# Performance work log

Measured on AMD Instinct MI355X. Metric: run time of the kernel, lower is better.

The kernel has to match this reference:

```python
import jax, jax.numpy as jnp
import numpy as np
import math

N_EMBD = 1024
N_HEAD = 16
BLOCK_SIZE = 2048
B, T = 2, 2048

def setup_inputs() -> dict:
    key = jax.random.key(0)
    ks = jax.random.split(key, 5)
    x = jax.random.normal(ks[0], (B, T, N_EMBD), dtype=jnp.float32)
    s = 1.0 / math.sqrt(N_EMBD)
    W_attn = jax.random.normal(ks[1], (N_EMBD, 3 * N_EMBD), dtype=jnp.float32) * s
    b_attn = jnp.zeros((3 * N_EMBD,), dtype=jnp.float32)
    W_proj = jax.random.normal(ks[2], (N_EMBD, N_EMBD), dtype=jnp.float32) * s
    b_proj = jnp.zeros((N_EMBD,), dtype=jnp.float32)
    return {"x": x, "W_attn": W_attn, "b_attn": b_attn, "W_proj": W_proj, "b_proj": b_proj}

def reference(x, W_attn, b_attn, W_proj, b_proj):
    Bx, Tx, C = x.shape
    hd = C // N_HEAD  # head dim
    a = x @ W_attn + b_attn                     # [B,T,3C]
    q, k, v = jnp.split(a, 3, axis=2)
    # [B,T,C] -> [B,H,T,hd]
    q = q.reshape(Bx, Tx, N_HEAD, hd).transpose(0, 2, 1, 3)
    k = k.reshape(Bx, Tx, N_HEAD, hd).transpose(0, 2, 1, 3)
    v = v.reshape(Bx, Tx, N_HEAD, hd).transpose(0, 2, 1, 3)
    # NOTE: nonstandard scale from the source: 1/sqrt(3*n_embd // n_head)
    scale = 1.0 / math.sqrt(C * 3 // N_HEAD)
    attn = jnp.einsum('bhqd,bhkd->bhqk', q, k) * scale
    causal = jnp.tril(jnp.ones((Tx, Tx), dtype=bool))
    attn = jnp.where(causal[None, None, :, :], attn, -jnp.inf)
    attn = jax.nn.softmax(attn, axis=-1)
    y = jnp.einsum('bhqk,bhkd->bhqd', attn, v)
    y = y.transpose(0, 2, 1, 3).reshape(Bx, Tx, C)
    return y @ W_proj + b_proj
```

## Files before the change

### kernel.cpp

```cpp
#include <hip/hip_runtime.h>
#include <hip/hip_bf16.h>

typedef unsigned short u16;
typedef __attribute__((ext_vector_type(8))) short frag8;
typedef __attribute__((ext_vector_type(4))) float f32x4;

#define DEV __device__ __forceinline__

DEV float b2f(u16 u) {
  unsigned int x = ((unsigned int)u) << 16;
  return __builtin_bit_cast(float, x);
}
DEV u16 f2b(float f) {
  unsigned int x = __builtin_bit_cast(unsigned int, f);
  x += 0x7fffu + ((x >> 16) & 1u);
  return (u16)(x >> 16);
}

DEV void gload_lds16(const u16* g, u16* l) {
  __builtin_amdgcn_global_load_lds(
      (const __attribute__((address_space(1))) unsigned int*)g,
      (__attribute__((address_space(3))) unsigned int*)l, 16, 0, 0);
}

__global__ void cvt_x(const float* __restrict__ x, u16* __restrict__ xb,
                      int n4) {
  int i = blockIdx.x * blockDim.x + threadIdx.x;
  if (i < n4) {
    float4 v = ((const float4*)x)[i];
    ushort4 o;
    o.x = f2b(v.x); o.y = f2b(v.y); o.z = f2b(v.z); o.w = f2b(v.w);
    ((ushort4*)xb)[i] = o;
  }
}

__global__ void cvt_wt(const float* __restrict__ W, u16* __restrict__ Wt,
                       int K, int N) {
  __shared__ u16 tile[32][33];
  const int nb = blockIdx.x * 32, kb = blockIdx.y * 32;
  const int tx = threadIdx.x, ty = threadIdx.y;
#pragma unroll
  for (int j = 0; j < 4; j++)
    tile[ty + j * 8][tx] = f2b(W[(size_t)(kb + ty + j * 8) * N + nb + tx]);
  __syncthreads();
#pragma unroll
  for (int j = 0; j < 4; j++)
    Wt[(size_t)(nb + ty + j * 8) * K + kb + tx] = tile[tx][ty + j * 8];
}

constexpr int BM = 128, BN = 128, BK = 32;

template <int MODE>
__launch_bounds__(256)
__global__ void gemm_bt(const u16* __restrict__ A, const u16* __restrict__ Bt,
                        const float* __restrict__ bias,
                        u16* __restrict__ o0, u16* __restrict__ o1,
                        u16* __restrict__ o2, float* __restrict__ of,
                        int M, int N, int K) {
  __shared__ __align__(16) u16 As[BM * BK];
  __shared__ __align__(16) u16 Bs[BN * BK];
  const int tid = threadIdx.x;
  const int lane = tid & 63;
  const int wid = tid >> 6;
  const int m0 = blockIdx.y * BM;
  const int n0 = blockIdx.x * BN;
  const int wm = (wid >> 1) * 64;
  const int wn = (wid & 1) * 64;

  f32x4 acc[4][4] = {};

  const int ldr0 = wid * 16 + (lane >> 2);
  const int ldr1 = ldr0 + 64;
  const int ldk = (lane & 3) * 8;
  const u16* Ag0 = A + (size_t)(m0 + ldr0) * K + ldk;
  const u16* Ag1 = A + (size_t)(m0 + ldr1) * K + ldk;
  const u16* Bg0 = Bt + (size_t)(n0 + ldr0) * K + ldk;
  const u16* Bg1 = Bt + (size_t)(n0 + ldr1) * K + ldk;
  u16* lA0 = &As[(wid * 16) * BK];
  u16* lA1 = &As[(wid * 16 + 64) * BK];
  u16* lB0 = &Bs[(wid * 16) * BK];
  u16* lB1 = &Bs[(wid * 16 + 64) * BK];

  const int lr = lane & 15, lg = lane >> 4;

  for (int k0 = 0; k0 < K; k0 += BK) {
    gload_lds16(Ag0 + k0, lA0);
    gload_lds16(Ag1 + k0, lA1);
    gload_lds16(Bg0 + k0, lB0);
    gload_lds16(Bg1 + k0, lB1);
    __syncthreads();
    frag8 af[4], bf[4];
#pragma unroll
    for (int i = 0; i < 4; i++) {
      af[i] = *(const frag8*)&As[(wm + i * 16 + lr) * BK + lg * 8];
      bf[i] = *(const frag8*)&Bs[(wn + i * 16 + lr) * BK + lg * 8];
    }
#pragma unroll
    for (int mi = 0; mi < 4; mi++)
#pragma unroll
      for (int ni = 0; ni < 4; ni++)
        acc[mi][ni] = __builtin_amdgcn_mfma_f32_16x16x32_bf16(
            af[mi], bf[ni], acc[mi][ni], 0, 0, 0);
    __syncthreads();
  }

#pragma unroll
  for (int ni = 0; ni < 4; ni++) {
    const int n = n0 + wn + ni * 16 + lr;
    const float bv = bias[n];
#pragma unroll
    for (int mi = 0; mi < 4; mi++) {
      const int mr = m0 + wm + mi * 16 + lg * 4;
#pragma unroll
      for (int r = 0; r < 4; r++) {
        const float v = acc[mi][ni][r] + bv;
        const int m = mr + r;
        if (MODE == 1) {
          of[(size_t)m * N + n] = v;
        } else {
          const int sec = n >> 10, c = n & 1023, hh = c >> 6, dd = c & 63;
          const int bb = m >> 11, tt = m & 2047;
          if (sec == 0)
            o0[(((size_t)bb * 16 + hh) * 2048 + tt) * 64 + dd] = f2b(v);
          else if (sec == 1)
            o1[(((size_t)bb * 16 + hh) * 2048 + tt) * 64 + dd] = f2b(v);
          else
            o2[(((size_t)bb * 16 + hh) * 64 + dd) * 2048 + tt] = f2b(v);
        }
      }
    }
  }
}

__launch_bounds__(256)
__global__ void attn_fwd(const u16* __restrict__ Qg, const u16* __restrict__ Kg,
                         const u16* __restrict__ Vtg, u16* __restrict__ Og) {
  __shared__ __align__(16) u16 Kl[2][4096];
  __shared__ __align__(16) u16 Vl[2][4096];
  __shared__ __align__(16) u16 P_lds[4][16][72];
  const int tid = threadIdx.x, lane = tid & 63, wid = tid >> 6;
  const int bid = blockIdx.x;
  const int hb = bid & 31;
  const int pa = bid >> 5;
  const int h = hb & 15, b = hb >> 4;
  const size_t bh = (size_t)b * 16 + h;
  const u16* Qp = Qg + bh * 2048 * 64;
  const u16* Kp = Kg + bh * 2048 * 64;
  const u16* Vp = Vtg + bh * 64 * 2048;
  const int lr = lane & 15, lg = lane >> 4;
  const float scale = 0.07216878364870322f;

  frag8 vone;
#pragma unroll
  for (int i = 0; i < 8; i++) vone[i] = (short)0x3F80;

  int srow[2], scol[2];
#pragma unroll
  for (int c = 0; c < 2; c++) {
    const int sb = c * 4096 + tid * 16;
    const int row = sb >> 7;
    const int cs = (sb >> 4) & 7;
    srow[c] = row;
    scol[c] = ((cs ^ (row & 7)) << 3);
  }
  const int ldsoff0 = wid * 512;
  const int ldsoff1 = 2048 + wid * 512;

  for (int ph = 0; ph < 2; ++ph) {
    const int qblk = ph ? (31 - pa) : pa;
    const int nkv = qblk + 1;
    const int q0 = qblk * 64 + wid * 16;

    frag8 qf[2];
#pragma unroll
    for (int ks = 0; ks < 2; ks++)
      qf[ks] = *(const frag8*)&Qp[(size_t)(q0 + lr) * 64 + ks * 32 + lg * 8];

    f32x4 o[4] = {};
    f32x4 ls = {};

    gload_lds16(Kp + (size_t)(0 + srow[0]) * 64 + scol[0], &Kl[0][ldsoff0]);
    gload_lds16(Kp + (size_t)(0 + srow[1]) * 64 + scol[1], &Kl[0][ldsoff1]);
    gload_lds16(Vp + (size_t)srow[0] * 2048 + 0 + scol[0], &Vl[0][ldsoff0]);
    gload_lds16(Vp + (size_t)srow[1] * 2048 + 0 + scol[1], &Vl[0][ldsoff1]);
    __syncthreads();

    for (int kt = 0; kt < nkv; ++kt) {
      const int cur = kt & 1;
      if (kt + 1 < nkv) {
        const int kv1 = (kt + 1) << 6;
        u16* Kd = Kl[cur ^ 1];
        u16* Vd = Vl[cur ^ 1];
        gload_lds16(Kp + (size_t)(kv1 + srow[0]) * 64 + scol[0], Kd + ldsoff0);
        gload_lds16(Kp + (size_t)(kv1 + srow[1]) * 64 + scol[1], Kd + ldsoff1);
        gload_lds16(Vp + (size_t)srow[0] * 2048 + kv1 + scol[0], Vd + ldsoff0);
        gload_lds16(Vp + (size_t)srow[1] * 2048 + kv1 + scol[1], Vd + ldsoff1);
      }
      const u16* Kc = Kl[cur];
      const u16* Vc = Vl[cur];
      f32x4 s[4] = {};
#pragma unroll
      for (int ks = 0; ks < 2; ks++)
#pragma unroll
        for (int ni = 0; ni < 4; ni++) {
          const frag8 kf = *(const frag8*)&Kc[(ni * 16 + lr) * 64 +
                                              (((ks * 4 + lg) ^ (lr & 7)) << 3)];
          s[ni] = __builtin_amdgcn_mfma_f32_16x16x32_bf16(qf[ks], kf, s[ni], 0,
                                                          0, 0);
        }
      const bool last = (kt == nkv - 1);
#pragma unroll
      for (int r = 0; r < 4; r++) {
#pragma unroll
        for (int ni = 0; ni < 4; ni++) {
          float sv = s[ni][r] * scale;
          if (last)
            sv = (ni * 16 + lr <= wid * 16 + lg * 4 + r) ? sv
                                                         : -__builtin_inff();
          P_lds[wid][lg * 4 + r][ni * 16 + lr] = f2b(__expf(sv));
        }
      }
      asm volatile("s_waitcnt lgkmcnt(0)" ::: "memory");
#pragma unroll
      for (int ks = 0; ks < 2; ks++) {
        const frag8 pf = *(const frag8*)&P_lds[wid][lr][ks * 32 + lg * 8];
        ls = __builtin_amdgcn_mfma_f32_16x16x32_bf16(pf, vone, ls, 0, 0, 0);
#pragma unroll
        for (int di = 0; di < 4; di++) {
          const frag8 vfr = *(const frag8*)&Vc[(di * 16 + lr) * 64 +
                                               (((ks * 4 + lg) ^ (lr & 7))
                                                << 3)];
          o[di] = __builtin_amdgcn_mfma_f32_16x16x32_bf16(pf, vfr, o[di], 0, 0,
                                                          0);
        }
      }
      __syncthreads();
    }

#pragma unroll
    for (int r = 0; r < 4; r++) {
      const int t = q0 + lg * 4 + r;
      const float inv = 1.f / ls[r];
#pragma unroll
      for (int di = 0; di < 4; di++) {
        const int col = (h << 6) + di * 16 + lr;
        Og[((size_t)b * 2048 + t) * 1024 + col] = f2b(o[di][r] * inv);
      }
    }
  }
}

extern "C" void kernel_launch(void* const* d_in, const int* in_sizes, int n_in,
                              void* d_out, int out_size, void* d_ws,
                              size_t ws_size, hipStream_t stream) {
  const float* x = (const float*)d_in[0];
  const float* Wa = (const float*)d_in[1];
  const float* ba = (const float*)d_in[2];
  const float* Wp = (const float*)d_in[3];
  const float* bp = (const float*)d_in[4];
  float* out = (float*)d_out;
  u16* ws = (u16*)d_ws;

  u16* WtA = ws;
  u16* WtP = WtA + (size_t)3072 * 1024;
  u16* Qb = WtP + (size_t)1024 * 1024;
  u16* Kb = Qb + (size_t)4194304;
  u16* Vt = Kb + (size_t)4194304;
  u16* Ob = Vt + (size_t)4194304;
  u16* xb = Ob + (size_t)4194304;

  cvt_x<<<4096, 256, 0, stream>>>(x, xb, 1048576);
  cvt_wt<<<dim3(96, 32), dim3(32, 8), 0, stream>>>(Wa, WtA, 1024, 3072);
  cvt_wt<<<dim3(32, 32), dim3(32, 8), 0, stream>>>(Wp, WtP, 1024, 1024);
  gemm_bt<0><<<dim3(24, 32), 256, 0, stream>>>(xb, WtA, ba, Qb, Kb, Vt,
                                               nullptr, 4096, 3072, 1024);
  attn_fwd<<<512, 256, 0, stream>>>(Qb, Kb, Vt, Ob);
  gemm_bt<1><<<dim3(8, 32), 256, 0, stream>>>(Ob, WtP, bp, nullptr, nullptr,
                                              nullptr, out, 4096, 1024, 1024);
}
```

Baseline: 201.9 us.

## Swizzle GEMM LDS layout, merge conversion kernels, add smaller-tile projection GEMM

Applies an XOR swizzle to the k-column chunk used for global-to-LDS loads and fragment reads in the GEMM, so that LDS reads hit fewer bank conflicts. Merges the three fp32-to-bf16 conversion launches into one kernel to cut launch overhead. Adds a dedicated output-projection GEMM with 64x128 tiles, which doubles the block count to 512 so more of the GPU is occupied. In exchange the projection tiles get less data reuse, and the merged kernel branches on block index.

```diff
diff --git a/kernel.cpp b/kernel.cpp
--- a/kernel.cpp
+++ b/kernel.cpp
@@ -23,22 +23,32 @@
       (__attribute__((address_space(3))) unsigned int*)l, 16, 0, 0);
 }
 
-__global__ void cvt_x(const float* __restrict__ x, u16* __restrict__ xb,
-                      int n4) {
-  int i = blockIdx.x * blockDim.x + threadIdx.x;
-  if (i < n4) {
+__global__ void cvt_all(const float* __restrict__ x, u16* __restrict__ xb,
+                        const float* __restrict__ Wa, u16* __restrict__ WtA,
+                        const float* __restrict__ Wp, u16* __restrict__ WtP) {
+  const int bid = blockIdx.x, tid = threadIdx.x;
+  if (bid < 4096) {
+    const int i = bid * 256 + tid;
     float4 v = ((const float4*)x)[i];
     ushort4 o;
     o.x = f2b(v.x); o.y = f2b(v.y); o.z = f2b(v.z); o.w = f2b(v.w);
     ((ushort4*)xb)[i] = o;
-  }
-}
-
-__global__ void cvt_wt(const float* __restrict__ W, u16* __restrict__ Wt,
-                       int K, int N) {
+    return;
+  }
   __shared__ u16 tile[32][33];
-  const int nb = blockIdx.x * 32, kb = blockIdx.y * 32;
-  const int tx = threadIdx.x, ty = threadIdx.y;
+  const float* W;
+  u16* Wt;
+  int nb, kb, K, N;
+  if (bid < 7168) {
+    const int b2 = bid - 4096;
+    W = Wa; Wt = WtA; K = 1024; N = 3072;
+    nb = (b2 % 96) * 32; kb = (b2 / 96) * 32;
+  } else {
+    const int b3 = bid - 7168;
+    W = Wp; Wt = WtP; K = 1024; N = 1024;
+    nb = (b3 % 32) * 32; kb = (b3 / 32) * 32;
+  }
+  const int tx = tid & 31, ty = tid >> 5;
 #pragma unroll
   for (int j = 0; j < 4; j++)
     tile[ty + j * 8][tx] = f2b(W[(size_t)(kb + ty + j * 8) * N + nb + tx]);
@@ -71,7 +81,8 @@
 
   const int ldr0 = wid * 16 + (lane >> 2);
   const int ldr1 = ldr0 + 64;
-  const int ldk = (lane & 3) * 8;
+  const int f0 = (lane >> 3) & 3;
+  const int ldk = (((lane & 3) ^ f0) << 3);
   const u16* Ag0 = A + (size_t)(m0 + ldr0) * K + ldk;
   const u16* Ag1 = A + (size_t)(m0 + ldr1) * K + ldk;
   const u16* Bg0 = Bt + (size_t)(n0 + ldr0) * K + ldk;
@@ -82,6 +93,8 @@
   u16* lB1 = &Bs[(wid * 16 + 64) * BK];
 
   const int lr = lane & 15, lg = lane >> 4;
+  const int fr = (lr >> 1) & 3;
+  const int rcol = ((lg ^ fr) << 3);
 
   for (int k0 = 0; k0 < K; k0 += BK) {
     gload_lds16(Ag0 + k0, lA0);
@@ -92,8 +105,8 @@
     frag8 af[4], bf[4];
 #pragma unroll
     for (int i = 0; i < 4; i++) {
-      af[i] = *(const frag8*)&As[(wm + i * 16 + lr) * BK + lg * 8];
-      bf[i] = *(const frag8*)&Bs[(wn + i * 16 + lr) * BK + lg * 8];
+      af[i] = *(const frag8*)&As[(wm + i * 16 + lr) * BK + rcol];
+      bf[i] = *(const frag8*)&Bs[(wn + i * 16 + lr) * BK + rcol];
     }
 #pragma unroll
     for (int mi = 0; mi < 4; mi++)
@@ -128,6 +141,71 @@
             o2[(((size_t)bb * 16 + hh) * 64 + dd) * 2048 + tt] = f2b(v);
         }
       }
+    }
+  }
+}
+
+__launch_bounds__(256)
+__global__ void gemm_proj(const u16* __restrict__ A, const u16* __restrict__ Bt,
+                          const float* __restrict__ bias,
+                          float* __restrict__ of, int M, int N, int K) {
+  __shared__ __align__(16) u16 As[64 * 32];
+  __shared__ __align__(16) u16 Bs[128 * 32];
+  const int tid = threadIdx.x;
+  const int lane = tid & 63;
+  const int wid = tid >> 6;
+  const int m0 = blockIdx.y * 64;
+  const int n0 = blockIdx.x * 128;
+  const int wm = (wid >> 1) * 32;
+  const int wn = (wid & 1) * 64;
+
+  f32x4 acc[2][4] = {};
+
+  const int srow = tid >> 2;
+  const int f0 = (srow >> 1) & 3;
+  const int scol = (((tid & 3) ^ f0) << 3);
+  const u16* Ag = A + (size_t)(m0 + srow) * K + scol;
+  const u16* Bg0 = Bt + (size_t)(n0 + srow) * K + scol;
+  const u16* Bg1 = Bt + (size_t)(n0 + srow + 64) * K + scol;
+  u16* lA = &As[wid * 512];
+  u16* lB0 = &Bs[wid * 512];
+  u16* lB1 = &Bs[2048 + wid * 512];
+
+  const int lr = lane & 15, lg = lane >> 4;
+  const int fr = (lr >> 1) & 3;
+  const int rcol = ((lg ^ fr) << 3);
+
+  for (int k0 = 0; k0 < K; k0 += 32) {
+    gload_lds16(Ag + k0, lA);
+    gload_lds16(Bg0 + k0, lB0);
+    gload_lds16(Bg1 + k0, lB1);
+    __syncthreads();
+    frag8 af[2], bf[4];
+#pragma unroll
+    for (int i = 0; i < 2; i++)
+      af[i] = *(const frag8*)&As[(wm + i * 16 + lr) * 32 + rcol];
+#pragma unroll
+    for (int i = 0; i < 4; i++)
+      bf[i] = *(const frag8*)&Bs[(wn + i * 16 + lr) * 32 + rcol];
+#pragma unroll
+    for (int mi = 0; mi < 2; mi++)
+#pragma unroll
+      for (int ni = 0; ni < 4; ni++)
+        acc[mi][ni] = __builtin_amdgcn_mfma_f32_16x16x32_bf16(
+            af[mi], bf[ni], acc[mi][ni], 0, 0, 0);
+    __syncthreads();
+  }
+
+#pragma unroll
+  for (int ni = 0; ni < 4; ni++) {
+    const int n = n0 + wn + ni * 16 + lr;
+    const float bv = bias[n];
+#pragma unroll
+    for (int mi = 0; mi < 2; mi++) {
+      const int mr = m0 + wm + mi * 16 + lg * 4;
+#pragma unroll
+      for (int r = 0; r < 4; r++)
+        of[(size_t)(mr + r) * N + n] = acc[mi][ni][r] + bv;
     }
   }
 }
@@ -269,12 +347,10 @@
   u16* Ob = Vt + (size_t)4194304;
   u16* xb = Ob + (size_t)4194304;
 
-  cvt_x<<<4096, 256, 0, stream>>>(x, xb, 1048576);
-  cvt_wt<<<dim3(96, 32), dim3(32, 8), 0, stream>>>(Wa, WtA, 1024, 3072);
-  cvt_wt<<<dim3(32, 32), dim3(32, 8), 0, stream>>>(Wp, WtP, 1024, 1024);
+  cvt_all<<<8192, 256, 0, stream>>>(x, xb, Wa, WtA, Wp, WtP);
   gemm_bt<0><<<dim3(24, 32), 256, 0, stream>>>(xb, WtA, ba, Qb, Kb, Vt,
                                                nullptr, 4096, 3072, 1024);
   attn_fwd<<<512, 256, 0, stream>>>(Qb, Kb, Vt, Ob);
-  gemm_bt<1><<<dim3(8, 32), 256, 0, stream>>>(Ob, WtP, bp, nullptr, nullptr,
-                                              nullptr, out, 4096, 1024, 1024);
-}
+  gemm_proj<<<dim3(8, 64), 256, 0, stream>>>(Ob, WtP, bp, out, 4096, 1024,
+                                             1024);
+}
```

Measured after the change: 189.7 us. 6.0% less time.
